# Optimization experiments

Measured on AMD Instinct MI355X. Metric: run time of the kernel, lower is better.

## Reference

```python
import jax, jax.numpy as jnp
import numpy as np

LN2 = 0.69314718056
N_RBF = 300  # np.arange(0, 30, 0.1)
D_MODEL = 256

def ssp(x):
    # shifted softplus: softplus(x) - ln(2)
    return jax.nn.softplus(x) - LN2

def setup_inputs() -> dict:
    key = jax.random.key(0)
    ks = jax.random.split(key, 12)
    B, S, D = 8, 256, D_MODEL
    s = lambda fan_in: 1.0 / np.sqrt(fan_in)
    return {
        "v": jax.random.normal(ks[0], (B, S, D), dtype=jnp.float32),
        "distance": jax.random.uniform(ks[1], (B, S, S), dtype=jnp.float32) * 10.0,
        "mask": jnp.ones((B, 1, 1, S), dtype=jnp.float32),
        "W_s1": jax.random.normal(ks[2], (N_RBF, 64), dtype=jnp.float32) * s(N_RBF),
        "b_s1": jnp.zeros((64,), dtype=jnp.float32),
        "W_s2": jax.random.normal(ks[3], (64, D), dtype=jnp.float32) * s(64),
        "b_s2": jnp.zeros((D,), dtype=jnp.float32),
        "W_a1": jax.random.normal(ks[4], (D, D), dtype=jnp.float32) * s(D),
        "b_a1": jnp.zeros((D,), dtype=jnp.float32),
        "W_a2": jax.random.normal(ks[5], (D, D), dtype=jnp.float32) * s(D),
        "b_a2": jnp.zeros((D,), dtype=jnp.float32),
        "W_a3": jax.random.normal(ks[6], (D, D), dtype=jnp.float32) * s(D),
        "b_a3": jnp.zeros((D,), dtype=jnp.float32),
    }

def reference(v, distance, mask, W_s1, b_s1, W_s2, b_s2, W_a1, b_a1, W_a2, b_a2, W_a3, b_a3):
    # mask: [B,1,1,S] -> [B,S,1]
    m = mask[:, 0, 0, :][..., None]
    v = v * m
    v = v @ W_a1 + b_a1          # atom_wise_1 (linear)
    v = v * m
    # RBF expansion: exp(-10 * (d - mu)^2), mu = 0.0, 0.1, ..., 29.9
    mu = jnp.arange(N_RBF, dtype=jnp.float32) * 0.1
    rbf = jnp.exp(-10.0 * jnp.square(distance[..., None] - mu))  # [B,S,S,300]
    h = ssp(rbf @ W_s1 + b_s1)   # [B,S,S,64]
    W = ssp(h @ W_s2 + b_s2)     # [B,S,S,D] continuous filter
    # v[B,1,S,D] * W[B,S,S,D], sum over axis=2 (sender j)
    v = jnp.einsum('bjd,bijd->bid', v, W)
    v = v * m
    v = ssp(v @ W_a2 + b_a2)
    v = v * m
    v = v @ W_a3 + b_a3
    v = v * m
    return v
```

## Files before the change

### kernel.cpp

```cpp
#include <hip/hip_runtime.h>
#include <hip/hip_bf16.h>
#include <cstdint>

#define LN2F 0.69314718056f

__device__ __forceinline__ float ssp(float x) {
    return fmaxf(x, 0.0f) + log1pf(expf(-fabsf(x))) - LN2F;
}

__device__ __forceinline__ uint16_t f2bf_rne(float x) {
    uint32_t u = __float_as_uint(x);
    u += 0x7FFF + ((u >> 16) & 1u);
    return (uint16_t)(u >> 16);
}

__device__ __forceinline__ float bf_lo(uint32_t u) { return __uint_as_float(u << 16); }
__device__ __forceinline__ float bf_hi(uint32_t u) { return __uint_as_float(u & 0xffff0000u); }

__global__ __launch_bounds__(512) void prep_kernel(
    const float* __restrict__ v, const float* __restrict__ mask,
    const float* __restrict__ W_a1, const float* __restrict__ b_a1,
    const float* __restrict__ W_s1, const float* __restrict__ b_s1,
    const float* __restrict__ W_s2, const float* __restrict__ b_s2,
    float* __restrict__ v1, uint16_t* __restrict__ T) {
    __shared__ float sA[8][304];
    __shared__ float sB[8][64];
    const int t = threadIdx.x;

    if (blockIdx.x < 256) {
        const int r0 = blockIdx.x * 8;
        for (int e = t; e < 2048; e += 512) {
            int row = e >> 8, c = e & 255;
            sA[row][c] = v[(r0 + row) * 256 + c];
        }
        __syncthreads();
        const int col = t & 255;
        const int g = t >> 8;
        const int c0 = blockIdx.x & 15;
        float acc[4] = {0.f, 0.f, 0.f, 0.f};
        float w[16], wn[16];
        {
            const int kt = c0 * 16;
            #pragma unroll
            for (int q = 0; q < 16; ++q) w[q] = W_a1[(kt + q) * 256 + col];
        }
        for (int i = 0; i < 16; ++i) {
            const int kt = ((c0 + i) & 15) * 16;
            if (i < 15) {
                const int ktn = ((c0 + i + 1) & 15) * 16;
                #pragma unroll
                for (int q = 0; q < 16; ++q) wn[q] = W_a1[(ktn + q) * 256 + col];
            }
            #pragma unroll
            for (int q4 = 0; q4 < 4; ++q4) {
                const int k = kt + q4 * 4;
                const float w0 = w[q4 * 4 + 0], w1 = w[q4 * 4 + 1];
                const float w2 = w[q4 * 4 + 2], w3 = w[q4 * 4 + 3];
                #pragma unroll
                for (int rr = 0; rr < 4; ++rr) {
                    const float4 xv = *(const float4*)&sA[g * 4 + rr][k];
                    float a = acc[rr];
                    a = fmaf(xv.x, w0, a);
                    a = fmaf(xv.y, w1, a);
                    a = fmaf(xv.z, w2, a);
                    a = fmaf(xv.w, w3, a);
                    acc[rr] = a;
                }
            }
            if (i < 15) {
                #pragma unroll
                for (int q = 0; q < 16; ++q) w[q] = wn[q];
            }
        }
        const float b = b_a1[col];
        #pragma unroll
        for (int rr = 0; rr < 4; ++rr) {
            const int r = r0 + g * 4 + rr;
            const float m = mask[r];
            v1[r * 256 + col] = (acc[rr] * m + b) * m;
        }
    } else {
        const int g0 = (blockIdx.x - 256) * 8;
        #pragma unroll
        for (int gg = 0; gg < 8; ++gg) {
            if (t < 300) {
                float d = (float)(g0 + gg) * 0.0025f;
                float diff = d - 0.1f * (float)t;
                sA[gg][t] = expf(-10.f * diff * diff);
            }
        }
        __syncthreads();
        {
            int gg = t >> 6, c = t & 63;
            float acc = b_s1[c];
            for (int r = 0; r < 300; ++r)
                acc = fmaf(sA[gg][r], W_s1[r * 64 + c], acc);
            sB[gg][c] = ssp(acc);
        }
        __syncthreads();
        {
            int col = t & 255, glo = t >> 8;
            float bb = b_s2[col];
            float val[4];
            #pragma unroll
            for (int q = 0; q < 4; ++q) val[q] = bb;
            for (int c = 0; c < 64; ++c) {
                float w = W_s2[c * 256 + col];
                #pragma unroll
                for (int q = 0; q < 4; ++q)
                    val[q] = fmaf(sB[glo + 2 * q][c], w, val[q]);
            }
            #pragma unroll
            for (int q = 0; q < 4; ++q) {
                int g = g0 + glo + 2 * q;
                T[g * 256 + col] = f2bf_rne(ssp(val[q]));
            }
        }
    }
}

__global__ __launch_bounds__(512) void main_kernel(
    const float* __restrict__ dist, const float* __restrict__ v1,
    const uint16_t* __restrict__ T, const float* __restrict__ mask,
    const float* __restrict__ W_a2, const float* __restrict__ b_a2,
    const float* __restrict__ W_a3, const float* __restrict__ b_a3,
    float* __restrict__ out) {
    __shared__ float v1s[32][256];
    __shared__ uint32_t sk[4][256];
    __shared__ float xs[4][256];
    const int t = threadIdx.x;
    const int r0 = blockIdx.x * 4;
    const int b = r0 >> 8;
    const int w = t >> 6;
    const int l = t & 63;
    const int row = w >> 1;
    const int d0 = ((w & 1) << 7) + (l << 1);

    #pragma unroll
    for (int it = 0; it < 2; ++it) {
        int e = t + it * 512;
        int rr = e >> 8, j = e & 255;
        float d = dist[(size_t)(r0 + rr) * 256 + j];
        int k = (int)fmaf(d, 400.f, 0.5f);
        sk[rr][j] = (uint32_t)(min(k, 4095) << 9);
    }

    float2 acc = make_float2(0.f, 0.f);
    const char* Tp = (const char*)T + (d0 << 1);
    const float4* srcbase = (const float4*)(v1 + ((size_t)b << 16));

    for (int jt = 0; jt < 256; jt += 32) {
        __syncthreads();
        const float4* src = srcbase + jt * 64;
        float4* dst = (float4*)v1s;
        #pragma unroll
        for (int u = 0; u < 4; ++u)
            dst[u * 512 + t] = src[u * 512 + t];
        __syncthreads();
        #pragma unroll 2
        for (int jj = 0; jj < 32; jj += 4) {
            const uint4 kk = *(const uint4*)&sk[row][jt + jj];
            const uint32_t u0 = *(const uint32_t*)(Tp + kk.x);
            const uint32_t u1 = *(const uint32_t*)(Tp + kk.y);
            const uint32_t u2 = *(const uint32_t*)(Tp + kk.z);
            const uint32_t u3 = *(const uint32_t*)(Tp + kk.w);
            const float2 w0 = *(const float2*)&v1s[jj + 0][d0];
            const float2 w1 = *(const float2*)&v1s[jj + 1][d0];
            const float2 w2 = *(const float2*)&v1s[jj + 2][d0];
            const float2 w3 = *(const float2*)&v1s[jj + 3][d0];
            acc.x = fmaf(bf_lo(u0), w0.x, acc.x);
            acc.y = fmaf(bf_hi(u0), w0.y, acc.y);
            acc.x = fmaf(bf_lo(u1), w1.x, acc.x);
            acc.y = fmaf(bf_hi(u1), w1.y, acc.y);
            acc.x = fmaf(bf_lo(u2), w2.x, acc.x);
            acc.y = fmaf(bf_hi(u2), w2.y, acc.y);
            acc.x = fmaf(bf_lo(u3), w3.x, acc.x);
            acc.y = fmaf(bf_hi(u3), w3.y, acc.y);
        }
    }
    __syncthreads();
    {
        const float m = mask[r0 + row];
        *(float2*)&xs[row][d0] = make_float2(acc.x * m, acc.y * m);
    }
    __syncthreads();

    const int col = t & 255;
    const int gg = t >> 8;
    const int rA = r0 + 2 * gg, rB = rA + 1;
    const int c0 = blockIdx.x & 15;

    float a0 = 0.f, a1 = 0.f;
    {
        float wv[16], wn[16];
        {
            const int kt = c0 * 16;
            #pragma unroll
            for (int q = 0; q < 16; ++q) wv[q] = W_a2[(kt + q) * 256 + col];
        }
        for (int i = 0; i < 16; ++i) {
            const int kt = ((c0 + i) & 15) * 16;
            if (i < 15) {
                const int ktn = ((c0 + i + 1) & 15) * 16;
                #pragma unroll
                for (int q = 0; q < 16; ++q) wn[q] = W_a2[(ktn + q) * 256 + col];
            }
            #pragma unroll
            for (int q4 = 0; q4 < 4; ++q4) {
                const int k = kt + (q4 << 2);
                const float4 xA = *(const float4*)&xs[2 * gg][k];
                const float4 xB = *(const float4*)&xs[2 * gg + 1][k];
                const float w0 = wv[q4 * 4 + 0], w1 = wv[q4 * 4 + 1];
                const float w2 = wv[q4 * 4 + 2], w3 = wv[q4 * 4 + 3];
                a0 = fmaf(xA.x, w0, a0); a0 = fmaf(xA.y, w1, a0);
                a0 = fmaf(xA.z, w2, a0); a0 = fmaf(xA.w, w3, a0);
                a1 = fmaf(xB.x, w0, a1); a1 = fmaf(xB.y, w1, a1);
                a1 = fmaf(xB.z, w2, a1); a1 = fmaf(xB.w, w3, a1);
            }
            if (i < 15) {
                #pragma unroll
                for (int q = 0; q < 16; ++q) wv[q] = wn[q];
            }
        }
    }
    const float b2 = b_a2[col];
    const float y0 = ssp(a0 + b2) * mask[rA];
    const float y1 = ssp(a1 + b2) * mask[rB];
    __syncthreads();
    xs[2 * gg][col] = y0;
    xs[2 * gg + 1][col] = y1;
    __syncthreads();

    float c0a = 0.f, c1a = 0.f;
    {
        float wv[16], wn[16];
        {
            const int kt = c0 * 16;
            #pragma unroll
            for (int q = 0; q < 16; ++q) wv[q] = W_a3[(kt + q) * 256 + col];
        }
        for (int i = 0; i < 16; ++i) {
            const int kt = ((c0 + i) & 15) * 16;
            if (i < 15) {
                const int ktn = ((c0 + i + 1) & 15) * 16;
                #pragma unroll
                for (int q = 0; q < 16; ++q) wn[q] = W_a3[(ktn + q) * 256 + col];
            }
            #pragma unroll
            for (int q4 = 0; q4 < 4; ++q4) {
                const int k = kt + (q4 << 2);
                const float4 xA = *(const float4*)&xs[2 * gg][k];
                const float4 xB = *(const float4*)&xs[2 * gg + 1][k];
                const float w0 = wv[q4 * 4 + 0], w1 = wv[q4 * 4 + 1];
                const float w2 = wv[q4 * 4 + 2], w3 = wv[q4 * 4 + 3];
                c0a = fmaf(xA.x, w0, c0a); c0a = fmaf(xA.y, w1, c0a);
                c0a = fmaf(xA.z, w2, c0a); c0a = fmaf(xA.w, w3, c0a);
                c1a = fmaf(xB.x, w0, c1a); c1a = fmaf(xB.y, w1, c1a);
                c1a = fmaf(xB.z, w2, c1a); c1a = fmaf(xB.w, w3, c1a);
            }
            if (i < 15) {
                #pragma unroll
                for (int q = 0; q < 16; ++q) wv[q] = wn[q];
            }
        }
    }
    const float b3 = b_a3[col];
    out[(size_t)rA * 256 + col] = (c0a + b3) * mask[rA];
    out[(size_t)rB * 256 + col] = (c1a + b3) * mask[rB];
}

extern "C" void kernel_launch(void* const* d_in, const int* in_sizes, int n_in,
                              void* d_out, int out_size, void* d_ws, size_t ws_size,
                              hipStream_t stream) {
    const float* v    = (const float*)d_in[0];
    const float* dist = (const float*)d_in[1];
    const float* mask = (const float*)d_in[2];
    const float* W_s1 = (const float*)d_in[3];
    const float* b_s1 = (const float*)d_in[4];
    const float* W_s2 = (const float*)d_in[5];
    const float* b_s2 = (const float*)d_in[6];
    const float* W_a1 = (const float*)d_in[7];
    const float* b_a1 = (const float*)d_in[8];
    const float* W_a2 = (const float*)d_in[9];
    const float* b_a2 = (const float*)d_in[10];
    const float* W_a3 = (const float*)d_in[11];
    const float* b_a3 = (const float*)d_in[12];
    float* out = (float*)d_out;

    char* ws = (char*)d_ws;
    float*    v1 = (float*)(ws);
    uint16_t* T  = (uint16_t*)(ws + (2u << 20));

    prep_kernel<<<768, 512, 0, stream>>>(v, mask, W_a1, b_a1, W_s1, b_s1, W_s2, b_s2, v1, T);
    main_kernel<<<512, 512, 0, stream>>>(dist, v1, T, mask, W_a2, b_a2, W_a3, b_a3, out);
}
```

Measured before the change: 73.31 us.

## Double-buffer v1 tiles in shared memory and split W_s1 dot accumulators

The main kernel now prefetches the next 32-row v1 tile into registers while computing on the current one, then writes it into a second shared buffer, so there is one barrier per tile instead of two and global load latency can overlap the gather-FMA loop. Separately, the prep kernel's 300-term dot product uses four independent accumulators to break the serial FMA dependency chain. The cost is doubled shared memory for v1s (64KB) plus 16 extra registers for the prefetch, which may reduce occupancy.

Result: no change. 72.40 us (-1.2%).

```diff
diff --git a/kernel.cpp b/kernel.cpp
--- a/kernel.cpp
+++ b/kernel.cpp
@@ -92,10 +92,14 @@
         __syncthreads();
         {
             int gg = t >> 6, c = t & 63;
-            float acc = b_s1[c];
-            for (int r = 0; r < 300; ++r)
-                acc = fmaf(sA[gg][r], W_s1[r * 64 + c], acc);
-            sB[gg][c] = ssp(acc);
+            float a0 = 0.f, a1 = 0.f, a2 = 0.f, a3 = 0.f;
+            for (int r = 0; r < 300; r += 4) {
+                a0 = fmaf(sA[gg][r + 0], W_s1[(r + 0) * 64 + c], a0);
+                a1 = fmaf(sA[gg][r + 1], W_s1[(r + 1) * 64 + c], a1);
+                a2 = fmaf(sA[gg][r + 2], W_s1[(r + 2) * 64 + c], a2);
+                a3 = fmaf(sA[gg][r + 3], W_s1[(r + 3) * 64 + c], a3);
+            }
+            sB[gg][c] = ssp(b_s1[c] + ((a0 + a1) + (a2 + a3)));
         }
         __syncthreads();
         {
@@ -125,7 +129,7 @@
     const float* __restrict__ W_a2, const float* __restrict__ b_a2,
     const float* __restrict__ W_a3, const float* __restrict__ b_a3,
     float* __restrict__ out) {
-    __shared__ float v1s[32][256];
+    __shared__ float v1s[2][32][256];
     __shared__ uint32_t sk[4][256];
     __shared__ float xs[4][256];
     const int t = threadIdx.x;
@@ -149,14 +153,26 @@
     const char* Tp = (const char*)T + (d0 << 1);
     const float4* srcbase = (const float4*)(v1 + ((size_t)b << 16));
 
-    for (int jt = 0; jt < 256; jt += 32) {
-        __syncthreads();
-        const float4* src = srcbase + jt * 64;
-        float4* dst = (float4*)v1s;
+    {
+        const float4* src = srcbase;
+        float4* dst = (float4*)v1s[0];
         #pragma unroll
         for (int u = 0; u < 4; ++u)
             dst[u * 512 + t] = src[u * 512 + t];
-        __syncthreads();
+    }
+    __syncthreads();
+
+    for (int jt = 0; jt < 256; jt += 32) {
+        const int cur = (jt >> 5) & 1;
+        float4 pf[4];
+        const bool more = (jt + 32) < 256;
+        if (more) {
+            const float4* src = srcbase + (jt + 32) * 64;
+            #pragma unroll
+            for (int u = 0; u < 4; ++u)
+                pf[u] = src[u * 512 + t];
+        }
+        const float (*vt)[256] = v1s[cur];
         #pragma unroll 2
         for (int jj = 0; jj < 32; jj += 4) {
             const uint4 kk = *(const uint4*)&sk[row][jt + jj];
@@ -164,10 +180,10 @@
             const uint32_t u1 = *(const uint32_t*)(Tp + kk.y);
             const uint32_t u2 = *(const uint32_t*)(Tp + kk.z);
             const uint32_t u3 = *(const uint32_t*)(Tp + kk.w);
-            const float2 w0 = *(const float2*)&v1s[jj + 0][d0];
-            const float2 w1 = *(const float2*)&v1s[jj + 1][d0];
-            const float2 w2 = *(const float2*)&v1s[jj + 2][d0];
-            const float2 w3 = *(const float2*)&v1s[jj + 3][d0];
+            const float2 w0 = *(const float2*)&vt[jj + 0][d0];
+            const float2 w1 = *(const float2*)&vt[jj + 1][d0];
+            const float2 w2 = *(const float2*)&vt[jj + 2][d0];
+            const float2 w3 = *(const float2*)&vt[jj + 3][d0];
             acc.x = fmaf(bf_lo(u0), w0.x, acc.x);
             acc.y = fmaf(bf_hi(u0), w0.y, acc.y);
             acc.x = fmaf(bf_lo(u1), w1.x, acc.x);
@@ -177,8 +193,14 @@
             acc.x = fmaf(bf_lo(u3), w3.x, acc.x);
             acc.y = fmaf(bf_hi(u3), w3.y, acc.y);
         }
-    }
-    __syncthreads();
+        if (more) {
+            float4* dst = (float4*)v1s[cur ^ 1];
+            #pragma unroll
+            for (int u = 0; u < 4; ++u)
+                dst[u * 512 + t] = pf[u];
+        }
+        __syncthreads();
+    }
     {
         const float m = mask[r0 + row];
         *(float2*)&xs[row][d0] = make_float2(acc.x * m, acc.y * m);
```
